# Performance work log

Hardware: AMD Instinct MI355X
Metric: run time of the kernel (lower is better)

The kernel has to match this reference:

```python
import jax, jax.numpy as jnp
import numpy as np

D_FIELDS = 16
HIDDEN = 16
N_POINTS = 1_000_000


def setup_inputs() -> dict:
    key = jax.random.key(0)
    ks = jax.random.split(key, 7)
    x = jax.random.normal(ks[0], (1, 3, N_POINTS), dtype=jnp.float32)
    # stacked per-field Conv1d(k=1) weights: conv weight [out,in,1] -> matrix [out,in]
    W1 = jax.random.normal(ks[1], (D_FIELDS, HIDDEN, 3), dtype=jnp.float32) * 0.1
    b1 = jax.random.normal(ks[2], (D_FIELDS, HIDDEN), dtype=jnp.float32) * 0.1
    W2 = jax.random.normal(ks[3], (D_FIELDS, HIDDEN, HIDDEN), dtype=jnp.float32) * 0.1
    b2 = jax.random.normal(ks[4], (D_FIELDS, HIDDEN), dtype=jnp.float32) * 0.1
    W3 = jax.random.normal(ks[5], (D_FIELDS, 3, HIDDEN), dtype=jnp.float32) * 0.1
    b3 = jax.random.normal(ks[6], (D_FIELDS, 3), dtype=jnp.float32) * 0.1
    return {"x": x, "W1": W1, "b1": b1, "W2": W2, "b2": b2, "W3": W3, "b3": b3, "D": D_FIELDS}


def reference(x, W1, b1, W2, b2, W3, b3, D):
    # x: [1, 3, N]. Original loops d in range(D) applying field d's MLP to x and
    # concatenating along dim 0 -> [D, 3, N]. Fused here as batched GEMMs over d.
    xs = x[0]  # [3, N]
    h = jax.nn.relu(jnp.einsum('dhc,cn->dhn', W1, xs) + b1[:, :, None])      # [D,H,N]
    h = jax.nn.relu(jnp.einsum('dgh,dhn->dgn', W2, h) + b2[:, :, None])      # [D,H,N]
    out = jnp.einsum('doh,dhn->don', W3, h) + b3[:, :, None]                 # [D,3,N]
    return out
```

## Files before the change

### kernel.cpp

```cpp
#include <hip/hip_runtime.h>


#define MFMA16(a, b, c) __builtin_amdgcn_mfma_f32_16x16x16f16((a), (b), (c), 0, 0, 0)

#define TILES_PER_WAVE 4
#define WAVES_PER_BLOCK 4
#define PTS_PER_BLOCK (TILES_PER_WAVE * WAVES_PER_BLOCK * 16)

typedef __fp16 pk16x2 __attribute__((ext_vector_type(2)));
typedef _Float16 half4_t __attribute__((ext_vector_type(4)));
typedef float float4_t __attribute__((ext_vector_type(4)));

union H2I { pk16x2 h; int i; };
union Frag { half4_t v; int i[2]; };

__device__ __forceinline__ int pkrtz(float a, float b) {
    H2I u; u.h = __builtin_amdgcn_cvt_pkrtz(a, b); return u.i;
}

__global__ __launch_bounds__(256) void fields_fixedd_kernel(
    const float* __restrict__ x,
    const float* __restrict__ W1, const float* __restrict__ b1,
    const float* __restrict__ W2, const float* __restrict__ b2,
    const float* __restrict__ W3, const float* __restrict__ b3,
    float* __restrict__ out, int N)
{
    const int lane = threadIdx.x & 63;
    const int wave = threadIdx.x >> 6;
    const int q    = lane >> 4;
    const int n16  = lane & 15;

    const int d     = blockIdx.x & 15;
    const int chunk = blockIdx.x >> 4;
    const int base  = chunk * PTS_PER_BLOCK + wave * (TILES_PER_WAVE * 16);

    Frag a1, a2, a3;
    {
        const float* w1 = W1 + (d * 16 + n16) * 3;
        a1.v = (half4_t){(_Float16)w1[0], (_Float16)w1[1], (_Float16)w1[2],
                         (_Float16)0.f};
        const float4_t w2 = *(const float4_t*)(W2 + (d * 16 + n16) * 16 + q * 4);
        a2.v = (half4_t){(_Float16)w2.x, (_Float16)w2.y, (_Float16)w2.z,
                         (_Float16)w2.w};
        if (n16 < 3) {
            const float4_t w3 = *(const float4_t*)(W3 + (d * 3 + n16) * 16 + q * 4);
            a3.v = (half4_t){(_Float16)w3.x, (_Float16)w3.y, (_Float16)w3.z,
                             (_Float16)w3.w};
        } else {
            a3.i[0] = 0; a3.i[1] = 0;
        }
    }
    const float4_t bias1 = *(const float4_t*)(b1 + d * 16 + q * 4);
    const float4_t bias2 = *(const float4_t*)(b2 + d * 16 + q * 4);
    float4_t bias3 = (float4_t){0.f, 0.f, 0.f, 0.f};
    if (q == 0) {
        bias3.x = b3[d * 3 + 0];
        bias3.y = b3[d * 3 + 1];
        bias3.z = b3[d * 3 + 2];
    }

    Frag xf[TILES_PER_WAVE];
#pragma unroll
    for (int t = 0; t < TILES_PER_WAVE; ++t) {
        const int pt = base + t * 16 + n16;
        float x0 = 0.f, x1 = 0.f, x2 = 0.f;
        if (q == 0 && pt < N) {
            x0 = x[pt];
            x1 = x[(size_t)N + pt];
            x2 = x[2 * (size_t)N + pt];
        }
        xf[t].i[0] = pkrtz(x0, x1);
        xf[t].i[1] = pkrtz(x2, 0.f);
    }

    float* o0 = out + (size_t)(d * 3 + 0) * N;
    float* o1 = out + (size_t)(d * 3 + 1) * N;
    float* o2 = out + (size_t)(d * 3 + 2) * N;

#pragma unroll
    for (int t = 0; t < TILES_PER_WAVE; ++t) {
        float4_t acc = MFMA16(a1.v, xf[t].v, bias1);
        Frag bf;
        bf.i[0] = pkrtz(fmaxf(acc.x, 0.f), fmaxf(acc.y, 0.f));
        bf.i[1] = pkrtz(fmaxf(acc.z, 0.f), fmaxf(acc.w, 0.f));
        acc = MFMA16(a2.v, bf.v, bias2);
        Frag cf;
        cf.i[0] = pkrtz(fmaxf(acc.x, 0.f), fmaxf(acc.y, 0.f));
        cf.i[1] = pkrtz(fmaxf(acc.z, 0.f), fmaxf(acc.w, 0.f));
        acc = MFMA16(a3.v, cf.v, bias3);
        const int pt = base + t * 16 + n16;
        if (q == 0 && pt < N) {
            o0[pt] = acc.x;
            o1[pt] = acc.y;
            o2[pt] = acc.z;
        }
    }
}

extern "C" void kernel_launch(void* const* d_in, const int* in_sizes, int n_in,
                              void* d_out, int out_size, void* d_ws, size_t ws_size,
                              hipStream_t stream) {
    const float* x  = (const float*)d_in[0];
    const float* W1 = (const float*)d_in[1];
    const float* b1 = (const float*)d_in[2];
    const float* W2 = (const float*)d_in[3];
    const float* b2 = (const float*)d_in[4];
    const float* W3 = (const float*)d_in[5];
    const float* b3 = (const float*)d_in[6];
    float* out = (float*)d_out;

    const int N = in_sizes[0] / 3;
    const int chunks = (N + PTS_PER_BLOCK - 1) / PTS_PER_BLOCK;
    const int grid = chunks * 16;
    fields_fixedd_kernel<<<grid, 256, 0, stream>>>(x, W1, b1, W2, b2, W3, b3, out, N);
}
```

Baseline: 288.0 us.

## Process more tiles per wave with a bounds-check-free fast path

After: 292.7 us. No clear change (+1.6%).

```diff
diff --git a/kernel.cpp b/kernel.cpp
--- a/kernel.cpp
+++ b/kernel.cpp
@@ -3,9 +3,10 @@
 
 #define MFMA16(a, b, c) __builtin_amdgcn_mfma_f32_16x16x16f16((a), (b), (c), 0, 0, 0)
 
-#define TILES_PER_WAVE 4
+#define TILES_PER_WAVE 25
 #define WAVES_PER_BLOCK 4
-#define PTS_PER_BLOCK (TILES_PER_WAVE * WAVES_PER_BLOCK * 16)
+#define PTS_PER_WAVE (TILES_PER_WAVE * 16)
+#define PTS_PER_BLOCK (PTS_PER_WAVE * WAVES_PER_BLOCK)
 
 typedef __fp16 pk16x2 __attribute__((ext_vector_type(2)));
 typedef _Float16 half4_t __attribute__((ext_vector_type(4)));
@@ -18,7 +19,7 @@
     H2I u; u.h = __builtin_amdgcn_cvt_pkrtz(a, b); return u.i;
 }
 
-__global__ __launch_bounds__(256) void fields_fixedd_kernel(
+__global__ __launch_bounds__(256) void fields_r8_kernel(
     const float* __restrict__ x,
     const float* __restrict__ W1, const float* __restrict__ b1,
     const float* __restrict__ W2, const float* __restrict__ b2,
@@ -32,13 +33,13 @@
 
     const int d     = blockIdx.x & 15;
     const int chunk = blockIdx.x >> 4;
-    const int base  = chunk * PTS_PER_BLOCK + wave * (TILES_PER_WAVE * 16);
+    const int base  = chunk * PTS_PER_BLOCK + wave * PTS_PER_WAVE;
 
     Frag a1, a2, a3;
     {
         const float* w1 = W1 + (d * 16 + n16) * 3;
-        a1.v = (half4_t){(_Float16)w1[0], (_Float16)w1[1], (_Float16)w1[2],
-                         (_Float16)0.f};
+        a1.v = (half4_t){(_Float16)w1[0], (_Float16)w1[1],
+                         (_Float16)w1[2], (_Float16)0.f};
         const float4_t w2 = *(const float4_t*)(W2 + (d * 16 + n16) * 16 + q * 4);
         a2.v = (half4_t){(_Float16)w2.x, (_Float16)w2.y, (_Float16)w2.z,
                          (_Float16)w2.w};
@@ -59,40 +60,74 @@
         bias3.z = b3[d * 3 + 2];
     }
 
-    Frag xf[TILES_PER_WAVE];
+    const bool isq0 = (q == 0);
+
+    const float* xp0 = x + base + n16;
+    const float* xp1 = xp0 + N;
+    const float* xp2 = xp1 + N;
+    float* op0 = out + (size_t)(d * 3 + 0) * N + base + n16;
+    float* op1 = out + (size_t)(d * 3 + 1) * N + base + n16;
+    float* op2 = out + (size_t)(d * 3 + 2) * N + base + n16;
+
+    if (base + PTS_PER_WAVE <= N) {
 #pragma unroll
-    for (int t = 0; t < TILES_PER_WAVE; ++t) {
-        const int pt = base + t * 16 + n16;
-        float x0 = 0.f, x1 = 0.f, x2 = 0.f;
-        if (q == 0 && pt < N) {
-            x0 = x[pt];
-            x1 = x[(size_t)N + pt];
-            x2 = x[2 * (size_t)N + pt];
+        for (int t = 0; t < TILES_PER_WAVE; ++t) {
+            const int off = t * 16;
+            const float x0 = xp0[off];
+            const float x1 = xp1[off];
+            const float x2 = xp2[off];
+            const int p01 = pkrtz(x0, x1);
+            const int p2  = pkrtz(x2, 0.f);
+            Frag xf;
+            xf.i[0] = isq0 ? p01 : 0;
+            xf.i[1] = isq0 ? p2  : 0;
+
+            float4_t acc = MFMA16(a1.v, xf.v, bias1);
+            Frag bf;
+            bf.i[0] = pkrtz(fmaxf(acc.x, 0.f), fmaxf(acc.y, 0.f));
+            bf.i[1] = pkrtz(fmaxf(acc.z, 0.f), fmaxf(acc.w, 0.f));
+            acc = MFMA16(a2.v, bf.v, bias2);
+            Frag cf;
+            cf.i[0] = pkrtz(fmaxf(acc.x, 0.f), fmaxf(acc.y, 0.f));
+            cf.i[1] = pkrtz(fmaxf(acc.z, 0.f), fmaxf(acc.w, 0.f));
+            acc = MFMA16(a3.v, cf.v, bias3);
+            if (isq0) {
+                op0[off] = acc.x;
+                op1[off] = acc.y;
+                op2[off] = acc.z;
+            }
         }
-        xf[t].i[0] = pkrtz(x0, x1);
-        xf[t].i[1] = pkrtz(x2, 0.f);
-    }
+    } else {
+#pragma unroll 1
+        for (int t = 0; t < TILES_PER_WAVE; ++t) {
+            const int off = t * 16;
+            const int pt = base + off + n16;
+            float x0 = 0.f, x1 = 0.f, x2 = 0.f;
+            if (isq0 && pt < N) {
+                x0 = xp0[off];
+                x1 = xp1[off];
+                x2 = xp2[off];
+            }
+            Frag xf;
+            xf.i[0] = pkrtz(x0, x1);
+            xf.i[1] = pkrtz(x2, 0.f);
 
-    float* o0 = out + (size_t)(d * 3 + 0) * N;
-    float* o1 = out + (size_t)(d * 3 + 1) * N;
-    float* o2 = out + (size_t)(d * 3 + 2) * N;
+            float4_t acc = MFMA16(a1.v, xf.v, bias1);
+            Frag bf;
+            bf.i[0] = pkrtz(fmaxf(acc.x, 0.f), fmaxf(acc.y, 0.f));
+            bf.i[1] = pkrtz(fmaxf(acc.z, 0.f), fmaxf(acc.w, 0.f));
 
-#pragma unroll
-    for (int t = 0; t < TILES_PER_WAVE; ++t) {
-        float4_t acc = MFMA16(a1.v, xf[t].v, bias1);
-        Frag bf;
-        bf.i[0] = pkrtz(fmaxf(acc.x, 0.f), fmaxf(acc.y, 0.f));
-        bf.i[1] = pkrtz(fmaxf(acc.z, 0.f), fmaxf(acc.w, 0.f));
-        acc = MFMA16(a2.v, bf.v, bias2);
-        Frag cf;
-        cf.i[0] = pkrtz(fmaxf(acc.x, 0.f), fmaxf(acc.y, 0.f));
-        cf.i[1] = pkrtz(fmaxf(acc.z, 0.f), fmaxf(acc.w, 0.f));
-        acc = MFMA16(a3.v, cf.v, bias3);
-        const int pt = base + t * 16 + n16;
-        if (q == 0 && pt < N) {
-            o0[pt] = acc.x;
-            o1[pt] = acc.y;
-            o2[pt] = acc.z;
+            acc = MFMA16(a2.v, bf.v, bias2);
+            Frag cf;
+            cf.i[0] = pkrtz(fmaxf(acc.x, 0.f), fmaxf(acc.y, 0.f));
+            cf.i[1] = pkrtz(fmaxf(acc.z, 0.f), fmaxf(acc.w, 0.f));
+
+            acc = MFMA16(a3.v, cf.v, bias3);
+            if (isq0 && pt < N) {
+                op0[off] = acc.x;
+                op1[off] = acc.y;
+                op2[off] = acc.z;
+            }
         }
     }
 }
@@ -112,5 +147,5 @@
     const int N = in_sizes[0] / 3;
     const int chunks = (N + PTS_PER_BLOCK - 1) / PTS_PER_BLOCK;
     const int grid = chunks * 16;
-    fields_fixedd_kernel<<<grid, 256, 0, stream>>>(x, W1, b1, W2, b2, W3, b3, out, N);
+    fields_r8_kernel<<<grid, 256, 0, stream>>>(x, W1, b1, W2, b2, W3, b3, out, N);
 }
```

## Use all 64 lanes per wave via quad-packed tiles and merged layer-3 MFMA

Applied to the files above, without the earlier changes.

New measurement: 240.2 us. 16.6% less time.

```diff
diff --git a/kernel.cpp b/kernel.cpp
--- a/kernel.cpp
+++ b/kernel.cpp
@@ -3,9 +3,11 @@
 
 #define MFMA16(a, b, c) __builtin_amdgcn_mfma_f32_16x16x16f16((a), (b), (c), 0, 0, 0)
 
-#define TILES_PER_WAVE 4
+#define TPG 4
+#define NG 6
 #define WAVES_PER_BLOCK 4
-#define PTS_PER_BLOCK (TILES_PER_WAVE * WAVES_PER_BLOCK * 16)
+#define PTS_PER_WAVE (NG * 64)
+#define PTS_PER_BLOCK (PTS_PER_WAVE * WAVES_PER_BLOCK)
 
 typedef __fp16 pk16x2 __attribute__((ext_vector_type(2)));
 typedef _Float16 half4_t __attribute__((ext_vector_type(4)));
@@ -18,7 +20,14 @@
     H2I u; u.h = __builtin_amdgcn_cvt_pkrtz(a, b); return u.i;
 }
 
-__global__ __launch_bounds__(256) void fields_fixedd_kernel(
+__device__ __forceinline__ int pk_relu_pack(float a, float b) {
+    H2I u; u.h = __builtin_amdgcn_cvt_pkrtz(a, b);
+    const pk16x2 z = {(__fp16)0.f, (__fp16)0.f};
+    u.h = __builtin_elementwise_max(u.h, z);
+    return u.i;
+}
+
+__global__ __launch_bounds__(256, 6) void fields_r14_kernel(
     const float* __restrict__ x,
     const float* __restrict__ W1, const float* __restrict__ b1,
     const float* __restrict__ W2, const float* __restrict__ b2,
@@ -30,70 +39,108 @@
     const int q    = lane >> 4;
     const int n16  = lane & 15;
 
-    const int d     = blockIdx.x & 15;
-    const int chunk = blockIdx.x >> 4;
-    const int base  = chunk * PTS_PER_BLOCK + wave * (TILES_PER_WAVE * 16);
+    const int bid = blockIdx.x;
+    const int r   = bid & 7;
+    const int d   = (bid >> 3) & 15;
+    const int a   = bid >> 7;
+    const int chunk  = a * 8 + r;
+    const int chunks = (N + PTS_PER_BLOCK - 1) / PTS_PER_BLOCK;
+    if (chunk >= chunks) return;
 
-    Frag a1, a2, a3;
+    const int base = chunk * PTS_PER_BLOCK + wave * PTS_PER_WAVE;
+    const bool isq[TPG] = { q == 0, q == 1, q == 2, q == 3 };
+
+    Frag a1, a2, a3v[TPG];
     {
         const float* w1 = W1 + (d * 16 + n16) * 3;
-        a1.v = (half4_t){(_Float16)w1[0], (_Float16)w1[1], (_Float16)w1[2],
-                         (_Float16)0.f};
+        a1.v = (half4_t){(_Float16)w1[0], (_Float16)w1[1],
+                         (_Float16)w1[2], (_Float16)0.f};
         const float4_t w2 = *(const float4_t*)(W2 + (d * 16 + n16) * 16 + q * 4);
         a2.v = (half4_t){(_Float16)w2.x, (_Float16)w2.y, (_Float16)w2.z,
                          (_Float16)w2.w};
-        if (n16 < 3) {
-            const float4_t w3 = *(const float4_t*)(W3 + (d * 3 + n16) * 16 + q * 4);
-            a3.v = (half4_t){(_Float16)w3.x, (_Float16)w3.y, (_Float16)w3.z,
-                             (_Float16)w3.w};
-        } else {
-            a3.i[0] = 0; a3.i[1] = 0;
+#pragma unroll
+        for (int s = 0; s < TPG; ++s) {
+            const int m = n16 - 4 * s;
+            if (m >= 0 && m < 3) {
+                const float4_t w3 = *(const float4_t*)(W3 + (d * 3 + m) * 16 + q * 4);
+                a3v[s].v = (half4_t){(_Float16)w3.x, (_Float16)w3.y,
+                                     (_Float16)w3.z, (_Float16)w3.w};
+            } else {
+                a3v[s].i[0] = 0; a3v[s].i[1] = 0;
+            }
         }
     }
-    const float4_t bias1 = *(const float4_t*)(b1 + d * 16 + q * 4);
-    const float4_t bias2 = *(const float4_t*)(b2 + d * 16 + q * 4);
-    float4_t bias3 = (float4_t){0.f, 0.f, 0.f, 0.f};
-    if (q == 0) {
-        bias3.x = b3[d * 3 + 0];
-        bias3.y = b3[d * 3 + 1];
-        bias3.z = b3[d * 3 + 2];
+    const float4_t b1v = *(const float4_t*)(b1 + d * 16 + q * 4);
+    const float4_t b2v = *(const float4_t*)(b2 + d * 16 + q * 4);
+    const float4_t b3r = (float4_t){b3[d * 3 + 0], b3[d * 3 + 1],
+                                    b3[d * 3 + 2], 0.f};
+
+    const float* xp0 = x + base;
+    const float* xp1 = xp0 + N;
+    const float* xp2 = xp1 + N;
+    float* op0 = out + (size_t)(d * 3 + 0) * N + base;
+    float* op1 = out + (size_t)(d * 3 + 1) * N + base;
+    float* op2 = out + (size_t)(d * 3 + 2) * N + base;
+
+    int nvalid = (N - base) / 64;
+    if (nvalid > NG) nvalid = NG;
+
+    float rb[2][3];
+    if (0 < nvalid) {
+        rb[0][0] = xp0[lane];
+        rb[0][1] = xp1[lane];
+        rb[0][2] = xp2[lane];
+    }
+    if (1 < nvalid) {
+        rb[1][0] = xp0[lane + 64];
+        rb[1][1] = xp1[lane + 64];
+        rb[1][2] = xp2[lane + 64];
     }
 
-    Frag xf[TILES_PER_WAVE];
 #pragma unroll
-    for (int t = 0; t < TILES_PER_WAVE; ++t) {
-        const int pt = base + t * 16 + n16;
-        float x0 = 0.f, x1 = 0.f, x2 = 0.f;
-        if (q == 0 && pt < N) {
-            x0 = x[pt];
-            x1 = x[(size_t)N + pt];
-            x2 = x[2 * (size_t)N + pt];
+    for (int g = 0; g < NG; ++g) {
+        if (g >= nvalid) break;
+        const int b = g & 1;
+
+        const int p01 = pkrtz(rb[b][0], rb[b][1]);
+        const int p2  = pkrtz(rb[b][2], 0.f);
+
+        if (g + 2 < nvalid) {
+            rb[b][0] = xp0[lane + (g + 2) * 64];
+            rb[b][1] = xp1[lane + (g + 2) * 64];
+            rb[b][2] = xp2[lane + (g + 2) * 64];
         }
-        xf[t].i[0] = pkrtz(x0, x1);
-        xf[t].i[1] = pkrtz(x2, 0.f);
-    }
 
-    float* o0 = out + (size_t)(d * 3 + 0) * N;
-    float* o1 = out + (size_t)(d * 3 + 1) * N;
-    float* o2 = out + (size_t)(d * 3 + 2) * N;
+        Frag xf[TPG];
+#pragma unroll
+        for (int s = 0; s < TPG; ++s) {
+            xf[s].i[0] = isq[s] ? p01 : 0;
+            xf[s].i[1] = isq[s] ? p2  : 0;
+        }
 
+        float4_t acc[TPG];
 #pragma unroll
-    for (int t = 0; t < TILES_PER_WAVE; ++t) {
-        float4_t acc = MFMA16(a1.v, xf[t].v, bias1);
-        Frag bf;
-        bf.i[0] = pkrtz(fmaxf(acc.x, 0.f), fmaxf(acc.y, 0.f));
-        bf.i[1] = pkrtz(fmaxf(acc.z, 0.f), fmaxf(acc.w, 0.f));
-        acc = MFMA16(a2.v, bf.v, bias2);
-        Frag cf;
-        cf.i[0] = pkrtz(fmaxf(acc.x, 0.f), fmaxf(acc.y, 0.f));
-        cf.i[1] = pkrtz(fmaxf(acc.z, 0.f), fmaxf(acc.w, 0.f));
-        acc = MFMA16(a3.v, cf.v, bias3);
-        const int pt = base + t * 16 + n16;
-        if (q == 0 && pt < N) {
-            o0[pt] = acc.x;
-            o1[pt] = acc.y;
-            o2[pt] = acc.z;
+        for (int s = 0; s < TPG; ++s) acc[s] = MFMA16(a1.v, xf[s].v, b1v);
+        Frag hf[TPG];
+#pragma unroll
+        for (int s = 0; s < TPG; ++s) {
+            hf[s].i[0] = pk_relu_pack(acc[s].x, acc[s].y);
+            hf[s].i[1] = pk_relu_pack(acc[s].z, acc[s].w);
         }
+#pragma unroll
+        for (int s = 0; s < TPG; ++s) acc[s] = MFMA16(a2.v, hf[s].v, b2v);
+#pragma unroll
+        for (int s = 0; s < TPG; ++s) {
+            hf[s].i[0] = pk_relu_pack(acc[s].x, acc[s].y);
+            hf[s].i[1] = pk_relu_pack(acc[s].z, acc[s].w);
+        }
+        float4_t o = b3r;
+#pragma unroll
+        for (int s = 0; s < TPG; ++s) o = MFMA16(a3v[s].v, hf[s].v, o);
+
+        op0[lane + g * 64] = o.x;
+        op1[lane + g * 64] = o.y;
+        op2[lane + g * 64] = o.z;
     }
 }
 
@@ -111,6 +158,7 @@
 
     const int N = in_sizes[0] / 3;
     const int chunks = (N + PTS_PER_BLOCK - 1) / PTS_PER_BLOCK;
-    const int grid = chunks * 16;
-    fields_fixedd_kernel<<<grid, 256, 0, stream>>>(x, W1, b1, W2, b2, W3, b3, out, N);
+    const int a_max  = (chunks + 7) / 8;
+    const int grid   = 8 * 16 * a_max;
+    fields_r14_kernel<<<grid, 256, 0, stream>>>(x, W1, b1, W2, b2, W3, b3, out, N);
 }
```
